# Kernel optimization log

Measured on AMD Instinct MI355X. Metric: run time of the kernel, lower is better.

Reference implementation:

```python
import jax, jax.numpy as jnp
import numpy as np

D_MODEL = 1024
N_HEADS = 16
D_FF = 4096
HEAD_DIM = D_MODEL // N_HEADS
EPS = 1e-5


def setup_inputs() -> dict:
    key = jax.random.key(0)
    ks = jax.random.split(key, 12)
    B, S, D = 2, 2048, D_MODEL
    s = 0.02
    return {
        "x": jax.random.normal(ks[0], (B, S, D), jnp.float32),
        "ln1_g": jnp.ones((D,), jnp.float32),
        "ln1_b": jnp.zeros((D,), jnp.float32),
        "qkv_w": jax.random.normal(ks[1], (3 * D, D), jnp.float32) * s,
        "qkv_b": jnp.zeros((3 * D,), jnp.float32),
        "out_w": jax.random.normal(ks[2], (D, D), jnp.float32) * s,
        "out_b": jnp.zeros((D,), jnp.float32),
        "ln2_g": jnp.ones((D,), jnp.float32),
        "ln2_b": jnp.zeros((D,), jnp.float32),
        "fc1_w": jax.random.normal(ks[3], (D_FF, D), jnp.float32) * s,
        "fc1_b": jnp.zeros((D_FF,), jnp.float32),
        "fc2_w": jax.random.normal(ks[4], (D, D_FF), jnp.float32) * s,
        "fc2_b": jnp.zeros((D,), jnp.float32),
    }


def _layernorm(x, g, b):
    mu = jnp.mean(x, axis=-1, keepdims=True)
    var = jnp.mean(jnp.square(x - mu), axis=-1, keepdims=True)
    return (x - mu) * jax.lax.rsqrt(var + EPS) * g + b


def _attention(h, qkv_w, qkv_b, out_w, out_b):
    B, S, D = h.shape
    qkv = h @ qkv_w.T + qkv_b  # [B,S,3D]
    q, k, v = jnp.split(qkv, 3, axis=-1)
    # [B,H,S,hd]
    q = q.reshape(B, S, N_HEADS, HEAD_DIM).transpose(0, 2, 1, 3)
    k = k.reshape(B, S, N_HEADS, HEAD_DIM).transpose(0, 2, 1, 3)
    v = v.reshape(B, S, N_HEADS, HEAD_DIM).transpose(0, 2, 1, 3)
    scale = HEAD_DIM ** -0.5
    scores = jnp.einsum("bhqd,bhkd->bhqk", q, k) * scale
    causal = jnp.tril(jnp.ones((S, S), bool))
    scores = jnp.where(causal, scores, -jnp.inf)
    attn = jax.nn.softmax(scores, axis=-1)
    out = jnp.einsum("bhqk,bhkd->bhqd", attn, v)
    out = out.transpose(0, 2, 1, 3).reshape(B, S, D)
    return out @ out_w.T + out_b


def reference(x, ln1_g, ln1_b, qkv_w, qkv_b, out_w, out_b,
              ln2_g, ln2_b, fc1_w, fc1_b, fc2_w, fc2_b):
    x = x + _attention(_layernorm(x, ln1_g, ln1_b), qkv_w, qkv_b, out_w, out_b)
    h = _layernorm(x, ln2_g, ln2_b)
    ff = jax.nn.gelu(h @ fc1_w.T + fc1_b, approximate=False) @ fc2_w.T + fc2_b
    return x + ff
```

## Files before the change

### kernel.cpp

```cpp
#include <hip/hip_runtime.h>
#include <stdint.h>

typedef uint16_t u16;
typedef uint32_t u32;
typedef __bf16 bf16_t;
typedef bf16_t bf16x8 __attribute__((ext_vector_type(8)));
typedef float f32x4 __attribute__((ext_vector_type(4)));
typedef u16 u16x4 __attribute__((ext_vector_type(4)));
typedef u16 u16x8 __attribute__((ext_vector_type(8)));

__device__ __forceinline__ float bf2f(u16 v) {
    union { u32 u; float f; } x; x.u = ((u32)v) << 16; return x.f;
}
__device__ __forceinline__ u16 f2bf(float f) {
    union { float f; u32 u; } x; x.f = f;
    u32 r = (x.u + 0x7fffu + ((x.u >> 16) & 1u)) >> 16;
    return (u16)r;
}

__device__ __forceinline__ void gload_lds16(const u16* g, u16* l) {
    __builtin_amdgcn_global_load_lds(
        (const __attribute__((address_space(1))) void*)g,
        (__attribute__((address_space(3))) void*)l,
        16, 0, 0);
}
#define WAIT_ALL() __builtin_amdgcn_s_waitcnt(0)
#define WAITVM(n) __builtin_amdgcn_s_waitcnt(0x0F70 | (n))
#define WAIT_LGKM0() __builtin_amdgcn_s_waitcnt(0xC07F)
#define BARRIER() __builtin_amdgcn_s_barrier()

__global__ __launch_bounds__(256) void cvt4_kernel(
    const float* __restrict__ s0, const float* __restrict__ s1,
    const float* __restrict__ s2, const float* __restrict__ s3,
    u16* __restrict__ d0, u16* __restrict__ d1,
    u16* __restrict__ d2, u16* __restrict__ d3)
{
    int i = blockIdx.x * 256 + threadIdx.x;
    const float* s; u16* d; int off;
    if (i < 786432)       { s = s0; d = d0; off = i; }
    else if (i < 1048576) { s = s1; d = d1; off = i - 786432; }
    else if (i < 2097152) { s = s2; d = d2; off = i - 1048576; }
    else                  { s = s3; d = d3; off = i - 2097152; }
    f32x4 v = ((const f32x4*)s)[off];
    u16x4 o;
#pragma unroll
    for (int j = 0; j < 4; j++) o[j] = f2bf(v[j]);
    ((u16x4*)d)[off] = o;
}

__global__ __launch_bounds__(256) void ln_kernel(
    const float* __restrict__ x, const float* __restrict__ g,
    const float* __restrict__ b, u16* __restrict__ out)
{
    const int row = blockIdx.x;
    const int tid = threadIdx.x;
    f32x4 xv = *(const f32x4*)(x + (size_t)row * 1024 + tid * 4);
    float v[4];
    float s = 0.f, s2 = 0.f;
#pragma unroll
    for (int i = 0; i < 4; i++) { v[i] = xv[i]; s += v[i]; s2 += v[i] * v[i]; }
#pragma unroll
    for (int off = 1; off < 64; off <<= 1) {
        s  += __shfl_xor(s, off);
        s2 += __shfl_xor(s2, off);
    }
    __shared__ float ws1[4], ws2[4];
    if ((tid & 63) == 0) { ws1[tid >> 6] = s; ws2[tid >> 6] = s2; }
    __syncthreads();
    s  = ws1[0] + ws1[1] + ws1[2] + ws1[3];
    s2 = ws2[0] + ws2[1] + ws2[2] + ws2[3];
    float mu  = s * (1.0f / 1024.0f);
    float var = s2 * (1.0f / 1024.0f) - mu * mu;
    float rstd = rsqrtf(var + 1e-5f);
    f32x4 gv = *(const f32x4*)(g + tid * 4);
    f32x4 bv = *(const f32x4*)(b + tid * 4);
    u16x4 ov;
#pragma unroll
    for (int i = 0; i < 4; i++)
        ov[i] = f2bf((v[i] - mu) * rstd * gv[i] + bv[i]);
    *(u16x4*)(out + (size_t)row * 1024 + tid * 4) = ov;
}

__global__ __launch_bounds__(256, 2) void gemm_bt(
    const u16* __restrict__ A, const u16* __restrict__ Bt,
    const float* __restrict__ bias, const float* res,
    void* C, int N, int K, int lda, int gelu)
{
    __shared__ __align__(16) u16 sA[2][128 * 32];
    __shared__ __align__(16) u16 sB[2][128 * 32];
    const int tid  = threadIdx.x;
    const int wave = tid >> 6, lane = tid & 63;
    const int lm = lane & 15, quad = lane >> 4;
    const int wm = wave >> 1, wn = wave & 1;
    const int row0 = blockIdx.y * 128, col0 = blockIdx.x * 128;
    const int r16 = lane >> 2;
    const int c8  = (lane & 3) * 8;
    const int niter = K >> 5;

    const u16* gsrc;
    size_t gstride;
    int chunk0;
    if (wave < 2) {
        chunk0 = wave * 4;
        gsrc = A + (size_t)(row0 + chunk0 * 16 + r16) * lda + c8;
        gstride = lda;
    } else {
        chunk0 = (wave - 2) * 4;
        gsrc = Bt + (size_t)(col0 + chunk0 * 16 + r16) * K + c8;
        gstride = K;
    }
    u16* lbase0 = (wave < 2) ? &sA[0][chunk0 * 512] : &sB[0][chunk0 * 512];
    u16* lbase1 = (wave < 2) ? &sA[1][chunk0 * 512] : &sB[1][chunk0 * 512];

    f32x4 acc[4][4];
#pragma unroll
    for (int i = 0; i < 4; i++)
#pragma unroll
        for (int j = 0; j < 4; j++) acc[i][j] = f32x4{0.f, 0.f, 0.f, 0.f};

#pragma unroll
    for (int j = 0; j < 4; j++)
        gload_lds16(gsrc + (size_t)(j * 16) * gstride, lbase0 + j * 512);

    for (int k = 0; k < niter; k++) {
        const int cur = k & 1;
        if (k + 1 < niter) {
            const u16* gs = gsrc + (size_t)(k + 1) * 32;
            u16* lb = cur ? lbase0 : lbase1;
#pragma unroll
            for (int j = 0; j < 4; j++)
                gload_lds16(gs + (size_t)(j * 16) * gstride, lb + j * 512);
            WAITVM(4);
        } else {
            WAITVM(0);
        }
        BARRIER();

        bf16x8 af[4], bfr[4];
#pragma unroll
        for (int t = 0; t < 4; t++)
            af[t] = *(const bf16x8*)&sA[cur][(wm * 64 + t * 16 + lm) * 32 + quad * 8];
#pragma unroll
        for (int t = 0; t < 4; t++)
            bfr[t] = *(const bf16x8*)&sB[cur][(wn * 64 + t * 16 + lm) * 32 + quad * 8];
#pragma unroll
        for (int i = 0; i < 4; i++)
#pragma unroll
            for (int j = 0; j < 4; j++)
                acc[i][j] = __builtin_amdgcn_mfma_f32_16x16x32_bf16(af[i], bfr[j], acc[i][j], 0, 0, 0);

        BARRIER();
    }

    float bj[4];
#pragma unroll
    for (int j = 0; j < 4; j++) bj[j] = bias[col0 + wn * 64 + j * 16 + lm];
#pragma unroll
    for (int i = 0; i < 4; i++) {
        int rbase = row0 + wm * 64 + i * 16 + quad * 4;
#pragma unroll
        for (int j = 0; j < 4; j++) {
            int c = col0 + wn * 64 + j * 16 + lm;
#pragma unroll
            for (int r = 0; r < 4; r++) {
                float v = acc[i][j][r] + bj[j];
                if (gelu) v = 0.5f * v * (1.0f + erff(v * 0.70710678118f));
                size_t idx = (size_t)(rbase + r) * N + c;
                if (res) {
                    ((float*)C)[idx] = v + res[idx];
                } else {
                    ((u16*)C)[idx] = f2bf(v);
                }
            }
        }
    }
}

__global__ __launch_bounds__(256, 2) void gemm_bt64(
    const u16* __restrict__ A, const u16* __restrict__ Bt,
    const float* __restrict__ bias, const float* res,
    void* C, int N, int K, int lda, int gelu)
{
    __shared__ __align__(16) u16 sA[2][128 * 32];
    __shared__ __align__(16) u16 sB[2][64 * 32];
    const int tid  = threadIdx.x;
    const int wave = tid >> 6, lane = tid & 63;
    const int lm = lane & 15, quad = lane >> 4;
    const int wm = wave >> 1, wn = wave & 1;
    const int row0 = blockIdx.y * 128, col0 = blockIdx.x * 64;
    const int r16 = lane >> 2;
    const int c8  = (lane & 3) * 8;
    const int niter = K >> 5;

    const u16* gs_[3];
    u16* lb0_[3];
    u16* lb1_[3];
#pragma unroll
    for (int j = 0; j < 3; j++) {
        int cid = wave * 3 + j;
        if (cid < 8) {
            gs_[j] = A + (size_t)(row0 + cid * 16 + r16) * lda + c8;
            lb0_[j] = &sA[0][cid * 512];
            lb1_[j] = &sA[1][cid * 512];
        } else {
            int bc = cid - 8;
            gs_[j] = Bt + (size_t)(col0 + bc * 16 + r16) * K + c8;
            lb0_[j] = &sB[0][bc * 512];
            lb1_[j] = &sB[1][bc * 512];
        }
    }
    const size_t gstride_a = lda, gstride_b = K;
    (void)gstride_a; (void)gstride_b;

    f32x4 acc[4][2];
#pragma unroll
    for (int i = 0; i < 4; i++)
#pragma unroll
        for (int j = 0; j < 2; j++) acc[i][j] = f32x4{0.f, 0.f, 0.f, 0.f};

#pragma unroll
    for (int j = 0; j < 3; j++) gload_lds16(gs_[j], lb0_[j]);

    for (int k = 0; k < niter; k++) {
        const int cur = k & 1;
        if (k + 1 < niter) {
#pragma unroll
            for (int j = 0; j < 3; j++)
                gload_lds16(gs_[j] + (size_t)(k + 1) * 32, cur ? lb0_[j] : lb1_[j]);
            WAITVM(3);
        } else {
            WAITVM(0);
        }
        BARRIER();

        bf16x8 af[4], bfr[2];
#pragma unroll
        for (int t = 0; t < 4; t++)
            af[t] = *(const bf16x8*)&sA[cur][(wm * 64 + t * 16 + lm) * 32 + quad * 8];
#pragma unroll
        for (int t = 0; t < 2; t++)
            bfr[t] = *(const bf16x8*)&sB[cur][(wn * 32 + t * 16 + lm) * 32 + quad * 8];
#pragma unroll
        for (int i = 0; i < 4; i++)
#pragma unroll
            for (int j = 0; j < 2; j++)
                acc[i][j] = __builtin_amdgcn_mfma_f32_16x16x32_bf16(af[i], bfr[j], acc[i][j], 0, 0, 0);

        BARRIER();
    }

    float bj[2];
#pragma unroll
    for (int j = 0; j < 2; j++) bj[j] = bias[col0 + wn * 32 + j * 16 + lm];
#pragma unroll
    for (int i = 0; i < 4; i++) {
        int rbase = row0 + wm * 64 + i * 16 + quad * 4;
#pragma unroll
        for (int j = 0; j < 2; j++) {
            int c = col0 + wn * 32 + j * 16 + lm;
#pragma unroll
            for (int r = 0; r < 4; r++) {
                float v = acc[i][j][r] + bj[j];
                if (gelu) v = 0.5f * v * (1.0f + erff(v * 0.70710678118f));
                size_t idx = (size_t)(rbase + r) * N + c;
                if (res) {
                    ((float*)C)[idx] = v + res[idx];
                } else {
                    ((u16*)C)[idx] = f2bf(v);
                }
            }
        }
    }
}

__global__ __launch_bounds__(256, 3) void attn_kernel(u16* qkv)
{
    __shared__ __align__(16) u16 sQ[64 * 64];
    __shared__ __align__(16) u16 sK[2][64 * 64];
    __shared__ __align__(16) u16 sVT[2][64 * 64];
    __shared__ __align__(16) u16 sP[4 * 16 * 72];

    const int tid  = threadIdx.x;
    const int wave = tid >> 6, lane = tid & 63;
    const int lm = lane & 15, quad = lane >> 4;
    int xi = blockIdx.x;
    int qz = (xi & 1) ? (31 - (xi >> 1)) : (xi >> 1);
    int qi = ((blockIdx.y >> 3) & 1) ? (31 - qz) : qz;
    const int q0 = qi * 64;
    const int b = blockIdx.y >> 4, h = blockIdx.y & 15;
    const size_t tok0 = (size_t)b * 2048;
    const int qcol = h * 64, kcol = 1024 + h * 64, vcol = 2048 + h * 64;
    const int r8 = lane >> 3;
    const int c8s = (((lane & 7) ^ r8) << 3);

    const int vkey = tid >> 2;
    const int vq   = tid & 3;
    const int vdq  = vq * 16;
    const u16* vbase = qkv + (tok0 + vkey) * 3072 + vcol + vdq;

#pragma unroll
    for (int j = 0; j < 2; j++) {
        int chunk = wave * 2 + j;
        int r = chunk * 8 + r8;
        gload_lds16(qkv + (tok0 + q0 + r) * 3072 + qcol + c8s, &sQ[chunk * 512]);
    }
#pragma unroll
    for (int j = 0; j < 2; j++) {
        int chunk = wave * 2 + j;
        int r = chunk * 8 + r8;
        gload_lds16(qkv + (tok0 + r) * 3072 + kcol + c8s, &sK[0][chunk * 512]);
    }
    u16x8 va = *(const u16x8*)vbase;
    u16x8 vb = *(const u16x8*)(vbase + 8);
    WAITVM(4);
    BARRIER();

    bf16x8 aq[2];
#pragma unroll
    for (int kk = 0; kk < 2; kk++)
        aq[kk] = *(const bf16x8*)
            &sQ[(wave * 16 + lm) * 64 + (((kk * 4 + quad) ^ (lm & 7)) << 3)];

    f32x4 oacc[4];
    float mrun[4], lrun[4];
#pragma unroll
    for (int n = 0; n < 4; n++) oacc[n] = f32x4{0.f, 0.f, 0.f, 0.f};
#pragma unroll
    for (int r = 0; r < 4; r++) { mrun[r] = -1e30f; lrun[r] = 0.f; }

    u16* sPw = &sP[wave * 16 * 72];
    const int ntiles = qi + 1;

    for (int tk = 0; tk < ntiles; tk++) {
        const int cur = tk & 1;
        u16x8 na = va, nb = vb;
        if (tk + 1 < ntiles) {
            const int kb1 = (tk + 1) * 64;
#pragma unroll
            for (int j = 0; j < 2; j++) {
                int chunk = wave * 2 + j;
                int r = chunk * 8 + r8;
                gload_lds16(qkv + (tok0 + kb1 + r) * 3072 + kcol + c8s,
                            &sK[1 - cur][chunk * 512]);
            }
            const u16* vr = vbase + (size_t)kb1 * 3072;
            na = *(const u16x8*)vr;
            nb = *(const u16x8*)(vr + 8);
            WAITVM(4);
        } else {
            WAITVM(0);
        }
#pragma unroll
        for (int i = 0; i < 8; i++) {
            int d = vdq + i;
            sVT[cur][d * 64 + ((((vkey >> 3) ^ i ^ vq)) << 3) + (vkey & 7)] = va[i];
        }
#pragma unroll
        for (int i = 0; i < 8; i++) {
            int d = vdq + 8 + i;
            sVT[cur][d * 64 + ((((vkey >> 3) ^ i ^ vq)) << 3) + (vkey & 7)] = vb[i];
        }
        va = na; vb = nb;
        WAIT_LGKM0();
        BARRIER();

        const int kb = tk * 64;
        float sc[4][4];
#pragma unroll
        for (int n = 0; n < 4; n++) {
            f32x4 s = f32x4{0.f, 0.f, 0.f, 0.f};
#pragma unroll
            for (int kk = 0; kk < 2; kk++) {
                bf16x8 bk = *(const bf16x8*)
                    &sK[cur][(n * 16 + lm) * 64 + (((kk * 4 + quad) ^ (lm & 7)) << 3)];
                s = __builtin_amdgcn_mfma_f32_16x16x32_bf16(aq[kk], bk, s, 0, 0, 0);
            }
            int col  = kb + n * 16 + lm;
            int rowb = q0 + wave * 16 + quad * 4;
#pragma unroll
            for (int r = 0; r < 4; r++)
                sc[n][r] = (col <= rowb + r) ? s[r] * 0.125f : -1e30f;
        }
#pragma unroll
        for (int r = 0; r < 4; r++) {
            float mx = fmaxf(fmaxf(sc[0][r], sc[1][r]), fmaxf(sc[2][r], sc[3][r]));
#pragma unroll
            for (int off = 1; off < 16; off <<= 1) mx = fmaxf(mx, __shfl_xor(mx, off));
            float mnew  = fmaxf(mrun[r], mx);
            float alpha = __expf(mrun[r] - mnew);
            float sum = 0.f;
#pragma unroll
            for (int n = 0; n < 4; n++) {
                float p = __expf(sc[n][r] - mnew);
                sc[n][r] = p;
                sum += p;
            }
#pragma unroll
            for (int off = 1; off < 16; off <<= 1) sum += __shfl_xor(sum, off);
            lrun[r] = lrun[r] * alpha + sum;
            mrun[r] = mnew;
#pragma unroll
            for (int n = 0; n < 4; n++) oacc[n][r] *= alpha;
        }
#pragma unroll
        for (int n = 0; n < 4; n++)
#pragma unroll
            for (int r = 0; r < 4; r++)
                sPw[(quad * 4 + r) * 72 + n * 16 + lm] = f2bf(sc[n][r]);
        bf16x8 ap[2];
#pragma unroll
        for (int kk = 0; kk < 2; kk++)
            ap[kk] = *(const bf16x8*)&sPw[lm * 72 + kk * 32 + quad * 8];
#pragma unroll
        for (int n = 0; n < 4; n++)
#pragma unroll
            for (int kk = 0; kk < 2; kk++) {
                bf16x8 bv = *(const bf16x8*)
                    &sVT[cur][(n * 16 + lm) * 64 +
                              ((((kk * 4 + quad) ^ (lm & 7) ^ n)) << 3)];
                oacc[n] = __builtin_amdgcn_mfma_f32_16x16x32_bf16(ap[kk], bv, oacc[n], 0, 0, 0);
            }

        BARRIER();
    }

    {
        int rowb = q0 + wave * 16 + quad * 4;
#pragma unroll
        for (int r = 0; r < 4; r++) {
            float inv = 1.0f / lrun[r];
#pragma unroll
            for (int n = 0; n < 4; n++) {
                int d = n * 16 + lm;
                qkv[(tok0 + rowb + r) * 3072 + qcol + d] = f2bf(oacc[n][r] * inv);
            }
        }
    }
}

extern "C" void kernel_launch(void* const* d_in, const int* in_sizes, int n_in,
                              void* d_out, int out_size, void* d_ws, size_t ws_size,
                              hipStream_t stream)
{
    (void)in_sizes; (void)n_in; (void)out_size; (void)ws_size;
    const float* x    = (const float*)d_in[0];
    const float* ln1g = (const float*)d_in[1];
    const float* ln1b = (const float*)d_in[2];
    const float* qkvwF= (const float*)d_in[3];
    const float* qkvb = (const float*)d_in[4];
    const float* outwF= (const float*)d_in[5];
    const float* outb = (const float*)d_in[6];
    const float* ln2g = (const float*)d_in[7];
    const float* ln2b = (const float*)d_in[8];
    const float* fc1wF= (const float*)d_in[9];
    const float* fc1b = (const float*)d_in[10];
    const float* fc2wF= (const float*)d_in[11];
    const float* fc2b = (const float*)d_in[12];
    float* out = (float*)d_out;
    u16*   ws  = (u16*)d_ws;
    const int M1 = 1 << 20;

    u16* qkvw = ws;
    u16* outw = ws + 3 * M1;
    u16* qkvB = ws + 4 * M1;
    u16* ff1  = ws;
    u16* fc1w = ws + 16 * M1;
    u16* fc2w = ws + 20 * M1;
    u16* h    = ws + 24 * M1;

    cvt4_kernel<<<12288, 256, 0, stream>>>(qkvwF, outwF, fc1wF, fc2wF,
                                           qkvw, outw, fc1w, fc2w);

    ln_kernel<<<4096, 256, 0, stream>>>(x, ln1g, ln1b, h);
    gemm_bt<<<dim3(24, 32), 256, 0, stream>>>(h, qkvw, qkvb, nullptr, qkvB,
                                              3072, 1024, 1024, 0);
    attn_kernel<<<dim3(32, 32), 256, 0, stream>>>(qkvB);
    gemm_bt64<<<dim3(16, 32), 256, 0, stream>>>(qkvB, outw, outb, x, out,
                                                1024, 1024, 3072, 0);
    ln_kernel<<<4096, 256, 0, stream>>>(out, ln2g, ln2b, h);
    gemm_bt<<<dim3(32, 32), 256, 0, stream>>>(h, fc1w, fc1b, nullptr, ff1,
                                              4096, 1024, 1024, 1);
    gemm_bt64<<<dim3(16, 32), 256, 0, stream>>>(ff1, fc2w, fc2b, out, out,
                                                1024, 4096, 4096, 0);
}
```

Measured before the change: 405.0 us.

## Compute transposed attention scores so softmax is per-lane, reuse Q LDS for P

Swaps the MFMA operand order so each lane holds one query row's scores, which turns the row max and sum reductions into two cross-quad shuffles instead of four 16-lane butterfly reductions per row. The running max and sum shrink from four registers to one per lane, and the per-row alpha and final l are redistributed with shuffles. The P scratch buffer is dropped and P is written, with an XOR swizzle, into the Q LDS region once Q is already in registers. Launch bounds are raised to four blocks per SM. The aim is less shuffle and VALU work plus lower LDS and register use for higher occupancy, at the cost of extra shuffles for alpha and l.

```diff
diff --git a/kernel.cpp b/kernel.cpp
--- a/kernel.cpp
+++ b/kernel.cpp
@@ -24,7 +24,6 @@
         (__attribute__((address_space(3))) void*)l,
         16, 0, 0);
 }
-#define WAIT_ALL() __builtin_amdgcn_s_waitcnt(0)
 #define WAITVM(n) __builtin_amdgcn_s_waitcnt(0x0F70 | (n))
 #define WAIT_LGKM0() __builtin_amdgcn_s_waitcnt(0xC07F)
 #define BARRIER() __builtin_amdgcn_s_barrier()
@@ -209,8 +208,6 @@
             lb1_[j] = &sB[1][bc * 512];
         }
     }
-    const size_t gstride_a = lda, gstride_b = K;
-    (void)gstride_a; (void)gstride_b;
 
     f32x4 acc[4][2];
 #pragma unroll
@@ -273,12 +270,11 @@
     }
 }
 
-__global__ __launch_bounds__(256, 3) void attn_kernel(u16* qkv)
-{
-    __shared__ __align__(16) u16 sQ[64 * 64];
+__global__ __launch_bounds__(256, 4) void attn_kernel(u16* qkv)
+{
+    __shared__ __align__(16) u16 sQP[64 * 64];
     __shared__ __align__(16) u16 sK[2][64 * 64];
     __shared__ __align__(16) u16 sVT[2][64 * 64];
-    __shared__ __align__(16) u16 sP[4 * 16 * 72];
 
     const int tid  = threadIdx.x;
     const int wave = tid >> 6, lane = tid & 63;
@@ -302,7 +298,7 @@
     for (int j = 0; j < 2; j++) {
         int chunk = wave * 2 + j;
         int r = chunk * 8 + r8;
-        gload_lds16(qkv + (tok0 + q0 + r) * 3072 + qcol + c8s, &sQ[chunk * 512]);
+        gload_lds16(qkv + (tok0 + q0 + r) * 3072 + qcol + c8s, &sQP[chunk * 512]);
     }
 #pragma unroll
     for (int j = 0; j < 2; j++) {
@@ -319,17 +315,16 @@
 #pragma unroll
     for (int kk = 0; kk < 2; kk++)
         aq[kk] = *(const bf16x8*)
-            &sQ[(wave * 16 + lm) * 64 + (((kk * 4 + quad) ^ (lm & 7)) << 3)];
+            &sQP[(wave * 16 + lm) * 64 + (((kk * 4 + quad) ^ (lm & 7)) << 3)];
 
     f32x4 oacc[4];
-    float mrun[4], lrun[4];
+    float mrun = -1e30f, lrun = 0.f;
 #pragma unroll
     for (int n = 0; n < 4; n++) oacc[n] = f32x4{0.f, 0.f, 0.f, 0.f};
-#pragma unroll
-    for (int r = 0; r < 4; r++) { mrun[r] = -1e30f; lrun[r] = 0.f; }
-
-    u16* sPw = &sP[wave * 16 * 72];
+
+    u16* sPw = &sQP[wave * 16 * 64];
     const int ntiles = qi + 1;
+    const int qrow_lane = q0 + wave * 16 + lm;
 
     for (int tk = 0; tk < ntiles; tk++) {
         const int cur = tk & 1;
@@ -371,46 +366,58 @@
             f32x4 s = f32x4{0.f, 0.f, 0.f, 0.f};
 #pragma unroll
             for (int kk = 0; kk < 2; kk++) {
-                bf16x8 bk = *(const bf16x8*)
+                bf16x8 ak = *(const bf16x8*)
                     &sK[cur][(n * 16 + lm) * 64 + (((kk * 4 + quad) ^ (lm & 7)) << 3)];
-                s = __builtin_amdgcn_mfma_f32_16x16x32_bf16(aq[kk], bk, s, 0, 0, 0);
-            }
-            int col  = kb + n * 16 + lm;
-            int rowb = q0 + wave * 16 + quad * 4;
-#pragma unroll
-            for (int r = 0; r < 4; r++)
-                sc[n][r] = (col <= rowb + r) ? s[r] * 0.125f : -1e30f;
-        }
-#pragma unroll
-        for (int r = 0; r < 4; r++) {
-            float mx = fmaxf(fmaxf(sc[0][r], sc[1][r]), fmaxf(sc[2][r], sc[3][r]));
-#pragma unroll
-            for (int off = 1; off < 16; off <<= 1) mx = fmaxf(mx, __shfl_xor(mx, off));
-            float mnew  = fmaxf(mrun[r], mx);
-            float alpha = __expf(mrun[r] - mnew);
-            float sum = 0.f;
-#pragma unroll
-            for (int n = 0; n < 4; n++) {
+                s = __builtin_amdgcn_mfma_f32_16x16x32_bf16(ak, aq[kk], s, 0, 0, 0);
+            }
+#pragma unroll
+            for (int r = 0; r < 4; r++) {
+                int key = kb + n * 16 + quad * 4 + r;
+                sc[n][r] = (key <= qrow_lane) ? s[r] * 0.125f : -1e30f;
+            }
+        }
+        float mx = sc[0][0];
+#pragma unroll
+        for (int n = 0; n < 4; n++)
+#pragma unroll
+            for (int r = 0; r < 4; r++) mx = fmaxf(mx, sc[n][r]);
+        mx = fmaxf(mx, __shfl_xor(mx, 16));
+        mx = fmaxf(mx, __shfl_xor(mx, 32));
+        float mnew  = fmaxf(mrun, mx);
+        float alpha = __expf(mrun - mnew);
+        float sum = 0.f;
+#pragma unroll
+        for (int n = 0; n < 4; n++)
+#pragma unroll
+            for (int r = 0; r < 4; r++) {
                 float p = __expf(sc[n][r] - mnew);
                 sc[n][r] = p;
                 sum += p;
             }
-#pragma unroll
-            for (int off = 1; off < 16; off <<= 1) sum += __shfl_xor(sum, off);
-            lrun[r] = lrun[r] * alpha + sum;
-            mrun[r] = mnew;
-#pragma unroll
-            for (int n = 0; n < 4; n++) oacc[n][r] *= alpha;
-        }
+        sum += __shfl_xor(sum, 16);
+        sum += __shfl_xor(sum, 32);
+        lrun = lrun * alpha + sum;
+        mrun = mnew;
+        float aT[4];
+#pragma unroll
+        for (int r = 0; r < 4; r++) aT[r] = __shfl(alpha, quad * 4 + r);
 #pragma unroll
         for (int n = 0; n < 4; n++)
 #pragma unroll
-            for (int r = 0; r < 4; r++)
-                sPw[(quad * 4 + r) * 72 + n * 16 + lm] = f2bf(sc[n][r]);
+            for (int r = 0; r < 4; r++) oacc[n][r] *= aT[r];
+#pragma unroll
+        for (int n = 0; n < 4; n++)
+#pragma unroll
+            for (int r = 0; r < 4; r++) {
+                int key = n * 16 + quad * 4 + r;
+                int addr = lm * 64 + (((key >> 3) ^ (lm & 7)) << 3) + (key & 7);
+                sPw[addr] = f2bf(sc[n][r]);
+            }
         bf16x8 ap[2];
 #pragma unroll
         for (int kk = 0; kk < 2; kk++)
-            ap[kk] = *(const bf16x8*)&sPw[lm * 72 + kk * 32 + quad * 8];
+            ap[kk] = *(const bf16x8*)
+                &sPw[lm * 64 + (((kk * 4 + quad) ^ (lm & 7)) << 3)];
 #pragma unroll
         for (int n = 0; n < 4; n++)
 #pragma unroll
@@ -425,10 +432,13 @@
     }
 
     {
+        float lT[4];
+#pragma unroll
+        for (int r = 0; r < 4; r++) lT[r] = __shfl(lrun, quad * 4 + r);
         int rowb = q0 + wave * 16 + quad * 4;
 #pragma unroll
         for (int r = 0; r < 4; r++) {
-            float inv = 1.0f / lrun[r];
+            float inv = 1.0f / lT[r];
 #pragma unroll
             for (int n = 0; n < 4; n++) {
                 int d = n * 16 + lm;
```

Result: faster. 368.0 us (-9.1%).
